# Performance work log

Hardware: AMD Instinct MI355X
Metric: run time of the kernel (lower is better)

The kernel has to match this reference:

```python
import jax, jax.numpy as jnp
from jax import lax
import numpy as np

NUM_LAYERS = 256
EPS = 1e-12


def setup_inputs() -> dict:
    key = jax.random.key(0)
    # values in [0.9, 1.1) so the 256-step multiplicative chain stays O(1)
    x = 0.9 + 0.2 * jax.random.uniform(key, (4, 19, 512, 512), dtype=jnp.float32)
    return {"x": x}


def _maxpool3x3_same(x):
    # torch MaxPool2d(kernel=3, stride=1, padding=1): pad value acts as -inf
    return lax.reduce_window(
        x, -jnp.inf, lax.max,
        window_dimensions=(1, 1, 3, 3),
        window_strides=(1, 1, 1, 1),
        padding=[(0, 0), (0, 0), (1, 1), (1, 1)],
    )


def reference(x):
    initial = x
    cur = -x
    one = jnp.float32(1.0)
    cur = cur.at[:, :, 0, :].set(one)
    cur = cur.at[:, :, -1, :].set(one)
    cur = cur.at[:, :, :, 0].set(one)
    cur = cur.at[:, :, :, -1].set(one)

    def step(c, _):
        return _maxpool3x3_same(c) * initial, None

    cur, _ = lax.scan(step, cur, None, length=NUM_LAYERS)
    # F.normalize default: L2 over dim=1, eps=1e-12
    norm = jnp.sqrt(jnp.sum(cur * cur, axis=1, keepdims=True))
    normed = cur / jnp.maximum(norm, EPS)
    return normed * initial
```

## Files before the change

kernel.cpp:

```cpp
#include <hip/hip_runtime.h>
#include <math.h>

#define BB 4
#define CC 19
#define HH 512
#define WW 512
#define NSLICE (BB * CC)
#define SLICE  (HH * WW)
#define W4     (WW / 4)
#define EPS    1e-12f
#define NEGINF (-INFINITY)

#define TSTEPS 16
#define NPASS  16

#define NBIG   512
#define NSMALL 192

#define TX   64
#define TY   8
#define COLS 8
#define THREADS 512

struct F8 { float4 a, b; };

__device__ __forceinline__ float dpp_up(float src) {
    int o = __builtin_amdgcn_update_dpp(__float_as_int(NEGINF), __float_as_int(src),
                                        0x138 , 0xF, 0xF, false);
    return __int_as_float(o);
}
__device__ __forceinline__ float dpp_dn(float src) {
    int o = __builtin_amdgcn_update_dpp(__float_as_int(NEGINF), __float_as_int(src),
                                        0x130 , 0xF, 0xF, false);
    return __int_as_float(o);
}

__global__ void init_kernel(const float* __restrict__ x, float* __restrict__ cur) {
    int t = blockIdx.x * blockDim.x + threadIdx.x;
    const float4* x4 = (const float4*)x;
    float4* c4 = (float4*)cur;
    float4 v = x4[t];
    int pix = t << 2;
    int s = pix & (SLICE - 1);
    int i = s >> 9;
    int j0 = s & 511;
    float4 o;
    o.x = -v.x; o.y = -v.y; o.z = -v.z; o.w = -v.w;
    if (i == 0 || i == HH - 1) {
        o.x = 1.0f; o.y = 1.0f; o.z = 1.0f; o.w = 1.0f;
    } else {
        if (j0 == 0)        o.x = 1.0f;
        if (j0 == WW - 4)   o.w = 1.0f;
    }
    c4[t] = o;
}

template<int R, int RR>
__device__ __forceinline__ void pass_body(const float* __restrict__ in,
                                          const float* __restrict__ xg,
                                          float* __restrict__ out,
                                          int bc, int tr0,
                                          float (&Tb)[2][TY][TX * 9],
                                          float (&Bb)[2][TY][TX * 9]) {
    const int tid  = threadIdx.x;
    const int tx   = tid & 63;
    const int ty   = tid >> 6;
    const int gstart = tr0 - TSTEPS;
    const int row0   = gstart + ty * R;
    const int col0   = tx * COLS;
    const size_t sbase = (size_t)bc * SLICE;

    const float4 neg4 = make_float4(NEGINF, NEGINF, NEGINF, NEGINF);
    const float4 one4 = make_float4(1.f, 1.f, 1.f, 1.f);

    float4 cl[R], cr[R], xl[R], xr_[R];

#pragma unroll
    for (int r = 0; r < R; ++r) {
        int grow = row0 + r;
        if (grow >= 0 && grow < HH) {
            const float4* p = (const float4*)(in + sbase + (size_t)grow * WW + col0);
            cl[r] = p[0]; cr[r] = p[1];
            const float4* q = (const float4*)(xg + sbase + (size_t)grow * WW + col0);
            xl[r] = q[0]; xr_[r] = q[1];
        } else {
            cl[r] = neg4; cr[r] = neg4; xl[r] = one4; xr_[r] = one4;
        }
    }

    auto hrow = [&](float4 a, float4 b) -> F8 {
        float lpx = dpp_up(b.w);
        float rpx = dpp_dn(a.x);
        F8 h;
        h.a.x = fmaxf(fmaxf(lpx, a.x), a.y);
        h.a.y = fmaxf(fmaxf(a.x, a.y), a.z);
        h.a.z = fmaxf(fmaxf(a.y, a.z), a.w);
        h.a.w = fmaxf(fmaxf(a.z, a.w), b.x);
        h.b.x = fmaxf(fmaxf(a.w, b.x), b.y);
        h.b.y = fmaxf(fmaxf(b.x, b.y), b.z);
        h.b.z = fmaxf(fmaxf(b.y, b.z), b.w);
        h.b.w = fmaxf(fmaxf(b.z, b.w), rpx);
        return h;
    };

    for (int t = 0; t < TSTEPS; ++t) {
        const int buf = t & 1;
        float* tp = &Tb[buf][ty][tx * 9];
        float* bp = &Bb[buf][ty][tx * 9];
        tp[0] = cl[0].x;      tp[1] = cl[0].y;      tp[2] = cl[0].z;      tp[3] = cl[0].w;
        tp[4] = cr[0].x;      tp[5] = cr[0].y;      tp[6] = cr[0].z;      tp[7] = cr[0].w;
        bp[0] = cl[R - 1].x;  bp[1] = cl[R - 1].y;  bp[2] = cl[R - 1].z;  bp[3] = cl[R - 1].w;
        bp[4] = cr[R - 1].x;  bp[5] = cr[R - 1].y;  bp[6] = cr[R - 1].z;  bp[7] = cr[R - 1].w;
        __syncthreads();

        float4 upA, upB, dnA, dnB;
        if (ty > 0) {
            const float* q = &Bb[buf][ty - 1][tx * 9];
            upA = make_float4(q[0], q[1], q[2], q[3]);
            upB = make_float4(q[4], q[5], q[6], q[7]);
        } else { upA = neg4; upB = neg4; }
        if (ty < TY - 1) {
            const float* q = &Tb[buf][ty + 1][tx * 9];
            dnA = make_float4(q[0], q[1], q[2], q[3]);
            dnB = make_float4(q[4], q[5], q[6], q[7]);
        } else { dnA = neg4; dnB = neg4; }

        F8 hA = hrow(upA, upB);
        F8 hB = hrow(cl[0], cr[0]);
#pragma unroll
        for (int r = 0; r < R; ++r) {
            F8 hC;
            if (r + 1 < R) hC = hrow(cl[r + 1], cr[r + 1]);
            else           hC = hrow(dnA, dnB);
            float4 vl, vr;
            vl.x = fmaxf(fmaxf(hA.a.x, hB.a.x), hC.a.x);
            vl.y = fmaxf(fmaxf(hA.a.y, hB.a.y), hC.a.y);
            vl.z = fmaxf(fmaxf(hA.a.z, hB.a.z), hC.a.z);
            vl.w = fmaxf(fmaxf(hA.a.w, hB.a.w), hC.a.w);
            vr.x = fmaxf(fmaxf(hA.b.x, hB.b.x), hC.b.x);
            vr.y = fmaxf(fmaxf(hA.b.y, hB.b.y), hC.b.y);
            vr.z = fmaxf(fmaxf(hA.b.z, hB.b.z), hC.b.z);
            vr.w = fmaxf(fmaxf(hA.b.w, hB.b.w), hC.b.w);
            cl[r].x = vl.x * xl[r].x;  cl[r].y = vl.y * xl[r].y;
            cl[r].z = vl.z * xl[r].z;  cl[r].w = vl.w * xl[r].w;
            cr[r].x = vr.x * xr_[r].x; cr[r].y = vr.y * xr_[r].y;
            cr[r].z = vr.z * xr_[r].z; cr[r].w = vr.w * xr_[r].w;
            hA = hB; hB = hC;
        }
#pragma unroll
        for (int r = 0; r < R; ++r) {
            int grow = row0 + r;
            if (grow < 0 || grow >= HH) { cl[r] = neg4; cr[r] = neg4; }
        }
    }

#pragma unroll
    for (int r = 0; r < R; ++r) {
        int a = ty * R + r;
        if (a >= TSTEPS && a < TSTEPS + RR) {
            int grow = row0 + r;
            float4* p = (float4*)(out + sbase + (size_t)grow * WW + col0);
            p[0] = cl[r]; p[1] = cr[r];
        }
    }
}

__global__ __launch_bounds__(THREADS, 1)
void pass_kernel(const float* __restrict__ in, const float* __restrict__ xg,
                 float* __restrict__ out) {
    __shared__ float Tb[2][TY][TX * 9];
    __shared__ float Bb[2][TY][TX * 9];

    const int bid = blockIdx.x;
    if (bid < NBIG) {
        const int g = (bid & 7) * (NBIG / 8) + (bid >> 3);
        int bc, tr0;
        if (g < 28 * 8) {
            bc  = g >> 3;
            tr0 = (g & 7) << 6;
        } else {
            int g2 = g - 28 * 8;
            bc  = 28 + g2 / 6;
            tr0 = (g2 % 6) << 6;
        }
        pass_body<12, 64>(in, xg, out, bc, tr0, Tb, Bb);
    } else {
        const int sb = bid - NBIG;
        const int h  = (sb & 7) * (NSMALL / 8) + (sb >> 3);
        const int bc  = 28 + (h >> 2);
        const int tr0 = 384 + ((h & 3) << 5);
        pass_body<8, 32>(in, xg, out, bc, tr0, Tb, Bb);
    }
}

__global__ void norm_kernel(const float* __restrict__ cur,
                            const float* __restrict__ x,
                            float* __restrict__ out) {
    int t = blockIdx.x * blockDim.x + threadIdx.x;
    int j4 = t & (W4 - 1);
    int i  = (t >> 7) & (HH - 1);
    int b  = t >> 16;
    size_t off = (size_t)b * CC * SLICE + (size_t)i * WW + (j4 << 2);

    float4 vals[CC];
    float sx = 0.f, sy = 0.f, sz = 0.f, sw = 0.f;
#pragma unroll
    for (int c = 0; c < CC; ++c) {
        float4 v = *(const float4*)(cur + off + (size_t)c * SLICE);
        vals[c] = v;
        sx += v.x * v.x; sy += v.y * v.y; sz += v.z * v.z; sw += v.w * v.w;
    }
    float4 r;
    r.x = 1.0f / fmaxf(sqrtf(sx), EPS);
    r.y = 1.0f / fmaxf(sqrtf(sy), EPS);
    r.z = 1.0f / fmaxf(sqrtf(sz), EPS);
    r.w = 1.0f / fmaxf(sqrtf(sw), EPS);
#pragma unroll
    for (int c = 0; c < CC; ++c) {
        float4 xv = *(const float4*)(x + off + (size_t)c * SLICE);
        float4 o;
        o.x = vals[c].x * xv.x * r.x;
        o.y = vals[c].y * xv.y * r.y;
        o.z = vals[c].z * xv.z * r.z;
        o.w = vals[c].w * xv.w * r.w;
        *(float4*)(out + off + (size_t)c * SLICE) = o;
    }
}

extern "C" void kernel_launch(void* const* d_in, const int* in_sizes, int n_in,
                              void* d_out, int out_size, void* d_ws, size_t ws_size,
                              hipStream_t stream) {
    const float* x = (const float*)d_in[0];
    float* out = (float*)d_out;
    float* ws  = (float*)d_ws;

    const int initBlocks = NSLICE * SLICE / 4 / 256;
    const int passBlocks = NBIG + NSMALL;
    const int normBlocks = BB * HH * W4 / 256;

    init_kernel<<<initBlocks, 256, 0, stream>>>(x, ws);
    float* a = ws;
    float* b = out;
    for (int it = 0; it < NPASS; ++it) {
        pass_kernel<<<passBlocks, THREADS, 0, stream>>>(a, x, b);
        float* tmp = a; a = b; b = tmp;
    }
    norm_kernel<<<normBlocks, 256, 0, stream>>>(ws, x, out);
}
```

Baseline: 2.074 ms.

## Use 16 wavefronts per block, re-read x from global each step

```diff
diff --git a/kernel.cpp b/kernel.cpp
--- a/kernel.cpp
+++ b/kernel.cpp
@@ -17,10 +17,9 @@
 #define NBIG   512
 #define NSMALL 192
 
-#define TX   64
-#define TY   8
+#define NW   16
 #define COLS 8
-#define THREADS 512
+#define THREADS 1024
 
 struct F8 { float4 a, b; };
 
@@ -60,32 +59,31 @@
                                           const float* __restrict__ xg,
                                           float* __restrict__ out,
                                           int bc, int tr0,
-                                          float (&Tb)[2][TY][TX * 9],
-                                          float (&Bb)[2][TY][TX * 9]) {
+                                          float4 (&Tb)[2][NW][2][64],
+                                          float4 (&Bb)[2][NW][2][64]) {
     const int tid  = threadIdx.x;
-    const int tx   = tid & 63;
-    const int ty   = tid >> 6;
+    const int lane = tid & 63;
+    const int w    = tid >> 6;
     const int gstart = tr0 - TSTEPS;
-    const int row0   = gstart + ty * R;
-    const int col0   = tx * COLS;
+    const int row0   = gstart + w * R;
+    const int col0   = lane * COLS;
     const size_t sbase = (size_t)bc * SLICE;
+    const float* xb = xg + sbase;
 
     const float4 neg4 = make_float4(NEGINF, NEGINF, NEGINF, NEGINF);
-    const float4 one4 = make_float4(1.f, 1.f, 1.f, 1.f);
-
-    float4 cl[R], cr[R], xl[R], xr_[R];
+
+    float4 cl[R], cr[R];
+    int xoff[R];
 
 #pragma unroll
     for (int r = 0; r < R; ++r) {
         int grow = row0 + r;
+        int gcl  = min(max(grow, 0), HH - 1);
+        xoff[r] = gcl * WW + col0;
         if (grow >= 0 && grow < HH) {
             const float4* p = (const float4*)(in + sbase + (size_t)grow * WW + col0);
             cl[r] = p[0]; cr[r] = p[1];
-            const float4* q = (const float4*)(xg + sbase + (size_t)grow * WW + col0);
-            xl[r] = q[0]; xr_[r] = q[1];
-        } else {
-            cl[r] = neg4; cr[r] = neg4; xl[r] = one4; xr_[r] = one4;
-        }
+        } else { cl[r] = neg4; cr[r] = neg4; }
     }
 
     auto hrow = [&](float4 a, float4 b) -> F8 {
@@ -105,24 +103,23 @@
 
     for (int t = 0; t < TSTEPS; ++t) {
         const int buf = t & 1;
-        float* tp = &Tb[buf][ty][tx * 9];
-        float* bp = &Bb[buf][ty][tx * 9];
-        tp[0] = cl[0].x;      tp[1] = cl[0].y;      tp[2] = cl[0].z;      tp[3] = cl[0].w;
-        tp[4] = cr[0].x;      tp[5] = cr[0].y;      tp[6] = cr[0].z;      tp[7] = cr[0].w;
-        bp[0] = cl[R - 1].x;  bp[1] = cl[R - 1].y;  bp[2] = cl[R - 1].z;  bp[3] = cl[R - 1].w;
-        bp[4] = cr[R - 1].x;  bp[5] = cr[R - 1].y;  bp[6] = cr[R - 1].z;  bp[7] = cr[R - 1].w;
+#pragma unroll
+        for (int r = 0; r < R; ++r) asm volatile("" : "+v"(xoff[r]));
+
+        Tb[buf][w][0][lane] = cl[0];
+        Tb[buf][w][1][lane] = cr[0];
+        Bb[buf][w][0][lane] = cl[R - 1];
+        Bb[buf][w][1][lane] = cr[R - 1];
         __syncthreads();
 
         float4 upA, upB, dnA, dnB;
-        if (ty > 0) {
-            const float* q = &Bb[buf][ty - 1][tx * 9];
-            upA = make_float4(q[0], q[1], q[2], q[3]);
-            upB = make_float4(q[4], q[5], q[6], q[7]);
+        if (w > 0) {
+            upA = Bb[buf][w - 1][0][lane];
+            upB = Bb[buf][w - 1][1][lane];
         } else { upA = neg4; upB = neg4; }
-        if (ty < TY - 1) {
-            const float* q = &Tb[buf][ty + 1][tx * 9];
-            dnA = make_float4(q[0], q[1], q[2], q[3]);
-            dnB = make_float4(q[4], q[5], q[6], q[7]);
+        if (w < NW - 1) {
+            dnA = Tb[buf][w + 1][0][lane];
+            dnB = Tb[buf][w + 1][1][lane];
         } else { dnA = neg4; dnB = neg4; }
 
         F8 hA = hrow(upA, upB);
@@ -132,6 +129,8 @@
             F8 hC;
             if (r + 1 < R) hC = hrow(cl[r + 1], cr[r + 1]);
             else           hC = hrow(dnA, dnB);
+            float4 xlv = *(const float4*)(xb + xoff[r]);
+            float4 xrv = *(const float4*)(xb + xoff[r] + 4);
             float4 vl, vr;
             vl.x = fmaxf(fmaxf(hA.a.x, hB.a.x), hC.a.x);
             vl.y = fmaxf(fmaxf(hA.a.y, hB.a.y), hC.a.y);
@@ -141,10 +140,10 @@
             vr.y = fmaxf(fmaxf(hA.b.y, hB.b.y), hC.b.y);
             vr.z = fmaxf(fmaxf(hA.b.z, hB.b.z), hC.b.z);
             vr.w = fmaxf(fmaxf(hA.b.w, hB.b.w), hC.b.w);
-            cl[r].x = vl.x * xl[r].x;  cl[r].y = vl.y * xl[r].y;
-            cl[r].z = vl.z * xl[r].z;  cl[r].w = vl.w * xl[r].w;
-            cr[r].x = vr.x * xr_[r].x; cr[r].y = vr.y * xr_[r].y;
-            cr[r].z = vr.z * xr_[r].z; cr[r].w = vr.w * xr_[r].w;
+            cl[r].x = vl.x * xlv.x;  cl[r].y = vl.y * xlv.y;
+            cl[r].z = vl.z * xlv.z;  cl[r].w = vl.w * xlv.w;
+            cr[r].x = vr.x * xrv.x;  cr[r].y = vr.y * xrv.y;
+            cr[r].z = vr.z * xrv.z;  cr[r].w = vr.w * xrv.w;
             hA = hB; hB = hC;
         }
 #pragma unroll
@@ -156,7 +155,7 @@
 
 #pragma unroll
     for (int r = 0; r < R; ++r) {
-        int a = ty * R + r;
+        int a = w * R + r;
         if (a >= TSTEPS && a < TSTEPS + RR) {
             int grow = row0 + r;
             float4* p = (float4*)(out + sbase + (size_t)grow * WW + col0);
@@ -165,11 +164,11 @@
     }
 }
 
-__global__ __launch_bounds__(THREADS, 1)
+__global__ __launch_bounds__(THREADS)
 void pass_kernel(const float* __restrict__ in, const float* __restrict__ xg,
                  float* __restrict__ out) {
-    __shared__ float Tb[2][TY][TX * 9];
-    __shared__ float Bb[2][TY][TX * 9];
+    __shared__ float4 Tb[2][NW][2][64];
+    __shared__ float4 Bb[2][NW][2][64];
 
     const int bid = blockIdx.x;
     if (bid < NBIG) {
@@ -183,13 +182,13 @@
             bc  = 28 + g2 / 6;
             tr0 = (g2 % 6) << 6;
         }
-        pass_body<12, 64>(in, xg, out, bc, tr0, Tb, Bb);
+        pass_body<6, 64>(in, xg, out, bc, tr0, Tb, Bb);
     } else {
         const int sb = bid - NBIG;
         const int h  = (sb & 7) * (NSMALL / 8) + (sb >> 3);
         const int bc  = 28 + (h >> 2);
         const int tr0 = 384 + ((h & 3) << 5);
-        pass_body<8, 32>(in, xg, out, bc, tr0, Tb, Bb);
+        pass_body<4, 32>(in, xg, out, bc, tr0, Tb, Bb);
     }
 }
 
```

Measured after the change: 2.691 ms. +29.8%, slower.
